# Kernel tuning notes

Measured on AMD Instinct MI355X. Metric: run time of the kernel, lower is better.

## Reference

```python
import jax, jax.numpy as jnp
import numpy as np

EPS_BN = 1e-5
EPS_ENT = 1e-15


def _gcn(x, src, dst, ew, W, b):
    # GCNConv: add self-loops (weight 1), symmetric deg^-1/2 normalization, aggregate x@W.
    n = x.shape[0]
    h = x @ W
    loop = jnp.arange(n)
    s2 = jnp.concatenate([src, loop])
    d2 = jnp.concatenate([dst, loop])
    we2 = jnp.concatenate([ew, jnp.ones((n,), x.dtype)])
    deg = jax.ops.segment_sum(we2, d2, num_segments=n)
    dinv = jnp.where(deg > 0, jax.lax.rsqrt(jnp.maximum(deg, 1e-12)), 0.0)
    coef = dinv[s2] * we2 * dinv[d2]
    return jax.ops.segment_sum(h[s2] * coef[:, None], d2, num_segments=n) + b


def _bn(x, g, be):
    # BatchNorm over the node dimension (training-mode batch stats)
    m = jnp.mean(x, axis=0)
    v = jnp.var(x, axis=0)
    return (x - m) * jax.lax.rsqrt(v + EPS_BN) * g + be


def _block(x, src, dst, ew, W, b, g, be):
    return jax.nn.silu(_bn(_gcn(x, src, dst, ew, W, b), g, be))


def _stoch_pool(x, src, dst, ew, Wp, bp, gp, bep):
    # DiffPool-style: soft cluster assignments from a ResidualBlock, pooled features/adjacency,
    # link loss ||A - S S^T||_F / N^2 (computed sparsely) and mean assignment entropy.
    n = x.shape[0]
    s = jax.nn.softmax(_block(x, src, dst, ew, Wp, bp, gp, bep), axis=-1)  # [n, K]
    K = s.shape[1]
    xp = s.T @ x  # [K, C]
    sw = s[src] * ew[:, None]  # [E, K]
    a_pool = sw.T @ s[dst]  # [K, K] = S^T A S
    cross = jnp.trace(a_pool)  # <A, S S^T>
    sts = s.T @ s  # [K, K]; ||S S^T||_F^2 = ||S^T S||_F^2
    link = jnp.sqrt(jnp.maximum(jnp.sum(ew * ew) - 2.0 * cross + jnp.sum(sts * sts), 0.0)) / (n * n)
    ent = jnp.mean(jnp.sum(-s * jnp.log(s + EPS_ENT), axis=-1))
    grid = jnp.arange(K)
    src_n = jnp.repeat(grid, K)
    dst_n = jnp.tile(grid, K)
    return xp, src_n, dst_n, a_pool.reshape(-1), link, ent


def _level(x, src, dst, ew, Wa, ba, ga, bea, Wb, bb, gb, beb, Wp, bp, gp, bep):
    x = _block(x, src, dst, ew, Wa, ba, ga, bea)
    x = x + _block(x, src, dst, ew, Wb, bb, gb, beb)  # pool_after-1 = 1 residual block
    return _stoch_pool(x, src, dst, ew, Wp, bp, gp, bep)


def setup_inputs() -> dict:
    key = jax.random.key(0)
    ks = jax.random.split(key, 10)
    N, E, IN, CH, K1, K2, OUT = 20000, 640000, 128, 128, 256, 64, 10
    lin = lambda k, fi, fo: (jax.random.normal(k, (fi, fo), jnp.float32) / np.sqrt(fi)).astype(jnp.float32)
    z = lambda c: jnp.zeros((c,), jnp.float32)
    o = lambda c: jnp.ones((c,), jnp.float32)
    d = {
        'x': jax.random.normal(ks[0], (N, IN), jnp.float32),
        'edge_index': jax.random.randint(ks[1], (2, E), 0, N, jnp.int32),
        'batch': jnp.zeros((N,), jnp.int32),
        'batch_ptr': jnp.array([0, N], jnp.int32),
        'W1a': lin(ks[2], IN, CH), 'b1a': z(CH), 'g1a': o(CH), 'be1a': z(CH),
        'W1b': lin(ks[3], CH, CH), 'b1b': z(CH), 'g1b': o(CH), 'be1b': z(CH),
        'Wp1': lin(ks[4], CH, K1), 'bp1': z(K1), 'gp1': o(K1), 'bep1': z(K1),
        'W2a': lin(ks[5], CH, CH), 'b2a': z(CH), 'g2a': o(CH), 'be2a': z(CH),
        'W2b': lin(ks[6], CH, CH), 'b2b': z(CH), 'g2b': o(CH), 'be2b': z(CH),
        'Wp2': lin(ks[7], CH, K2), 'bp2': z(K2), 'gp2': o(K2), 'bep2': z(K2),
        'Wlin': lin(ks[8], CH, OUT), 'blin': z(OUT),
    }
    return d


def reference(x, edge_index, batch, batch_ptr,
              W1a, b1a, g1a, be1a, W1b, b1b, g1b, be1b, Wp1, bp1, gp1, bep1,
              W2a, b2a, g2a, be2a, W2b, b2b, g2b, be2b, Wp2, bp2, gp2, bep2,
              Wlin, blin):
    src, dst = edge_index[0], edge_index[1]
    ew = jnp.ones(src.shape, x.dtype)  # level-1 edge_weight is None -> ones
    x, src, dst, ew, l1, e1 = _level(x, src, dst, ew, W1a, b1a, g1a, be1a,
                                     W1b, b1b, g1b, be1b, Wp1, bp1, gp1, bep1)
    x, src, dst, ew, l2, e2 = _level(x, src, dst, ew, W2a, b2a, g2a, be2a,
                                     W2b, b2b, g2b, be2b, Wp2, bp2, gp2, bep2)
    pooled = jnp.mean(x, axis=0, keepdims=True)  # global_mean_pool, single graph (B=1)
    logits = pooled @ Wlin + blin
    return jax.nn.log_softmax(logits, axis=1), (e1 + e2) + (l1 + l2)
```

## Files before the change

### kernel.cpp

```cpp
#include <hip/hip_runtime.h>

#define EPS_BN 1e-5f
typedef unsigned int uint;
typedef unsigned short ushort;
typedef __attribute__((ext_vector_type(8))) short bf16x8;
typedef __attribute__((ext_vector_type(4))) float f32x4;

__device__ inline ushort f2bf(float f) {
  uint u = __float_as_uint(f);
  uint r = (u + 0x7FFFu + ((u >> 16) & 1u)) >> 16;
  return (ushort)r;
}
__device__ inline float bflo(uint h) { return __uint_as_float(h << 16); }
__device__ inline float bfhi(uint h) { return __uint_as_float(h & 0xFFFF0000u); }


__global__ void k_pre(const int* __restrict__ dst, int* __restrict__ cnt, int E,
                      const float* __restrict__ x, ushort* __restrict__ xb, int n4, int HB) {
  int b = blockIdx.x;
  if (b < HB) {
    int e = b * 256 + threadIdx.x;
    if (e < E) atomicAdd(&cnt[dst[e]], 1);
  } else {
    int i = (b - HB) * 256 + threadIdx.x;
    if (i < n4) {
      float4 v = ((const float4*)x)[i];
      ushort4 o;
      o.x = f2bf(v.x); o.y = f2bf(v.y); o.z = f2bf(v.z); o.w = f2bf(v.w);
      ((ushort4*)xb)[i] = o;
    }
  }
}

__global__ __launch_bounds__(256) void k_scan_par(
    const int* __restrict__ cnt, int* __restrict__ rowptr, int* __restrict__ cursor,
    float* __restrict__ dinv, int* __restrict__ flags, int* __restrict__ partials,
    int N, int E) {
  __shared__ int wsum[4];
  __shared__ int sbase;
  int tile = blockIdx.x;
  int t = threadIdx.x;
  int lane = t & 63, w = t >> 6;
  int i0 = tile * 1024 + t * 4;
  int c[4];
#pragma unroll
  for (int j = 0; j < 4; ++j) {
    int i = i0 + j;
    c[j] = (i < N) ? cnt[i] : 0;
  }
  int p1 = c[0], p2 = p1 + c[1], p3 = p2 + c[2];
  int tsum = p3 + c[3];
  int incl = tsum;
  for (int o = 1; o < 64; o <<= 1) {
    int v = __shfl_up(incl, o);
    if (lane >= o) incl += v;
  }
  int excl = incl - tsum;
  if (lane == 63) wsum[w] = incl;
  __syncthreads();
  if (t == 0) {
    int tot = wsum[0] + wsum[1] + wsum[2] + wsum[3];
    int basev = 0;
    if (tile > 0) {
      while (atomicAdd(&flags[tile - 1], 0) == 0) {}
      basev = atomicAdd(&partials[tile - 1], 0);
    }
    atomicExch(&partials[tile], basev + tot);
    __threadfence();
    atomicExch(&flags[tile], 1);
    sbase = basev;
  }
  __syncthreads();
  int base = sbase;
  for (int ww = 0; ww < w; ++ww) base += wsum[ww];
  base += excl;
  int pre[4] = {0, p1, p2, p3};
#pragma unroll
  for (int j = 0; j < 4; ++j) {
    int i = i0 + j;
    if (i < N) {
      int run = base + pre[j];
      rowptr[i] = run; cursor[i] = run;
      dinv[i] = rsqrtf(1.0f + (float)c[j]);
    }
  }
  if (tile == 0 && t == 0) rowptr[N] = E;
}

__global__ void k_fill_csr(const int* __restrict__ key, const int* __restrict__ val,
                           int* __restrict__ cursor, int* __restrict__ col, int E) {
  int e = blockIdx.x * blockDim.x + threadIdx.x;
  if (e < E) {
    int pos = atomicAdd(&cursor[key[e]], 1);
    col[pos] = val[e];
  }
}


__global__ void k_gather_agg_b2(const int* __restrict__ rowptr, const int* __restrict__ col,
                                const float* __restrict__ dinv, const ushort* __restrict__ H,
                                float* __restrict__ out, int C2) {
  int d = blockIdx.x;
  int c2 = threadIdx.x;
  const uint* H2 = (const uint*)H;
  int b = rowptr[d], e = rowptr[d + 1];
  float a0 = 0.f, a1 = 0.f;
#pragma unroll 4
  for (int i = b; i < e; ++i) {
    int s = col[i];
    float dv = dinv[s];
    uint h = H2[(size_t)s * C2 + c2];
    a0 += dv * bflo(h);
    a1 += dv * bfhi(h);
  }
  float dd = dinv[d];
  uint hd = H2[(size_t)d * C2 + c2];
  float2 o;
  o.x = dd * a0 + dd * dd * bflo(hd);
  o.y = dd * a1 + dd * dd * bfhi(hd);
  *(float2*)(out + (size_t)d * (C2 * 2) + c2 * 2) = o;
}

__global__ void k_gather_agg_b2b(const int* __restrict__ rowptr, const int* __restrict__ col,
                                 const float* __restrict__ dinv, const ushort* __restrict__ H,
                                 ushort* __restrict__ out, int C2) {
  int d = blockIdx.x;
  int c2 = threadIdx.x;
  const uint* H2 = (const uint*)H;
  int b = rowptr[d], e = rowptr[d + 1];
  float a0 = 0.f, a1 = 0.f;
#pragma unroll 4
  for (int i = b; i < e; ++i) {
    int s = col[i];
    float dv = dinv[s];
    uint h = H2[(size_t)s * C2 + c2];
    a0 += dv * bflo(h);
    a1 += dv * bfhi(h);
  }
  float dd = dinv[d];
  uint hd = H2[(size_t)d * C2 + c2];
  ushort2 o;
  o.x = f2bf(dd * a0 + dd * dd * bflo(hd));
  o.y = f2bf(dd * a1 + dd * dd * bfhi(hd));
  *(ushort2*)(out + (size_t)d * (C2 * 2) + c2 * 2) = o;
}

__global__ void k_gather_T_b2b(const int* __restrict__ rowptr, const int* __restrict__ col,
                               const ushort* __restrict__ S, ushort* __restrict__ T, int C2) {
  int s = blockIdx.x;
  int c2 = threadIdx.x;
  const uint* S2 = (const uint*)S;
  int b = rowptr[s], e = rowptr[s + 1];
  float a0 = 0.f, a1 = 0.f;
#pragma unroll 4
  for (int i = b; i < e; ++i) {
    int d = col[i];
    uint h = S2[(size_t)d * C2 + c2];
    a0 += bflo(h);
    a1 += bfhi(h);
  }
  ushort2 o; o.x = f2bf(a0); o.y = f2bf(a1);
  *(ushort2*)(T + (size_t)s * (C2 * 2) + c2 * 2) = o;
}


__global__ void k_tconv(const float* __restrict__ in, ushort* __restrict__ out,
                        int R, int Cc) {
  __shared__ float tile[32][33];
  int c0 = blockIdx.x * 32, r0 = blockIdx.y * 32;
  int tx = threadIdx.x, ty = threadIdx.y;
  for (int i = 0; i < 32; i += 8) {
    int r = r0 + ty + i, c = c0 + tx;
    if (r < R && c < Cc) tile[ty + i][tx] = in[(size_t)r * Cc + c];
  }
  __syncthreads();
  for (int i = 0; i < 32; i += 8) {
    int oc = c0 + ty + i;
    int orr = r0 + tx;
    if (oc < Cc && orr < R) out[(size_t)oc * R + orr] = f2bf(tile[tx][ty + i]);
  }
}

__global__ void k_tconv_b(const ushort* __restrict__ in, ushort* __restrict__ out,
                          int R, int Cc) {
  __shared__ ushort tile[32][33];
  int c0 = blockIdx.x * 32, r0 = blockIdx.y * 32;
  int tx = threadIdx.x, ty = threadIdx.y;
  for (int i = 0; i < 32; i += 8) {
    int r = r0 + ty + i, c = c0 + tx;
    if (r < R && c < Cc) tile[ty + i][tx] = in[(size_t)r * Cc + c];
  }
  __syncthreads();
  for (int i = 0; i < 32; i += 8) {
    int oc = c0 + ty + i;
    int orr = r0 + tx;
    if (oc < Cc && orr < R) out[(size_t)oc * R + orr] = tile[tx][ty + i];
  }
}

__global__ void k_tconv3(const float* __restrict__ W0, const float* __restrict__ W1,
                         const float* __restrict__ W2,
                         ushort* __restrict__ O0, ushort* __restrict__ O1,
                         ushort* __restrict__ O2, int K1) {
  __shared__ float tile[32][33];
  int z = blockIdx.z;
  const float* in = (z == 0) ? W0 : (z == 1) ? W1 : W2;
  ushort* out = (z == 0) ? O0 : (z == 1) ? O1 : O2;
  int Cc = (z == 2) ? K1 : 128;
  int R = 128;
  int c0 = blockIdx.x * 32, r0 = blockIdx.y * 32;
  if (c0 >= Cc) return;
  int tx = threadIdx.x, ty = threadIdx.y;
  for (int i = 0; i < 32; i += 8) {
    int r = r0 + ty + i, c = c0 + tx;
    if (r < R && c < Cc) tile[ty + i][tx] = in[(size_t)r * Cc + c];
  }
  __syncthreads();
  for (int i = 0; i < 32; i += 8) {
    int oc = c0 + ty + i;
    int orr = r0 + tx;
    if (oc < Cc && orr < R) out[(size_t)oc * R + orr] = f2bf(tile[tx][ty + i]);
  }
}

__global__ __launch_bounds__(256) void k_mfma_nt(
    const ushort* __restrict__ A, const ushort* __restrict__ B, float* __restrict__ C,
    ushort* __restrict__ Cb, int I, int J, int K, int kChunk, int atom) {
  __shared__ ushort As[64][40];
  __shared__ ushort Bs[64][40];
  int t = threadIdx.x;
  int w = t >> 6, l = t & 63;
  int i0 = blockIdx.y * 64, j0 = blockIdx.x * 64;
  int k0 = blockIdx.z * kChunk;
  int k1 = min(k0 + kChunk, K);
  f32x4 acc[4] = {};
  int lrow = t >> 2;
  int lk = (t & 3) * 8;
  for (int kk = k0; kk < k1; kk += 32) {
    uint4 av = make_uint4(0u, 0u, 0u, 0u);
    int ar = i0 + lrow;
    if (ar < I) av = *(const uint4*)(A + (size_t)ar * K + kk + lk);
    uint4 bv = *(const uint4*)(B + (size_t)(j0 + lrow) * K + kk + lk);
    *(uint4*)&As[lrow][lk] = av;
    *(uint4*)&Bs[lrow][lk] = bv;
    __syncthreads();
    bf16x8 af = *(const bf16x8*)&As[16 * w + (l & 15)][(l >> 4) * 8];
#pragma unroll
    for (int jt = 0; jt < 4; ++jt) {
      bf16x8 bf = *(const bf16x8*)&Bs[16 * jt + (l & 15)][(l >> 4) * 8];
      acc[jt] = __builtin_amdgcn_mfma_f32_16x16x32_bf16(af, bf, acc[jt], 0, 0, 0);
    }
    __syncthreads();
  }
  int rbase = i0 + 16 * w + ((l >> 4) * 4);
  int cbase = j0 + (l & 15);
#pragma unroll
  for (int jt = 0; jt < 4; ++jt) {
#pragma unroll
    for (int rr = 0; rr < 4; ++rr) {
      int r = rbase + rr;
      if (r < I) {
        size_t idx = (size_t)r * J + jt * 16 + cbase;
        if (Cb) Cb[idx] = f2bf(acc[jt][rr]);
        else if (atom) atomicAdd(&C[idx], acc[jt][rr]);
        else C[idx] = acc[jt][rr];
      }
    }
  }
}

__global__ __launch_bounds__(256) void k_mfma3(
    const ushort* __restrict__ St, const ushort* __restrict__ ATSt,
    const ushort* __restrict__ R2t,
    float* __restrict__ apT, float* __restrict__ sts, float* __restrict__ xp,
    int K, int kChunk) {
  __shared__ ushort As[64][40];
  __shared__ ushort Bs[64][40];
  int xb_ = blockIdx.x;
  const ushort* B; float* C; int J, j0;
  if (xb_ < 4)      { B = ATSt; C = apT; J = 256; j0 = xb_ * 64; }
  else if (xb_ < 8) { B = St;   C = sts; J = 256; j0 = (xb_ - 4) * 64; }
  else              { B = R2t;  C = xp;  J = 128; j0 = (xb_ - 8) * 64; }
  int t = threadIdx.x;
  int w = t >> 6, l = t & 63;
  int i0 = blockIdx.y * 64;
  int k0 = blockIdx.z * kChunk;
  int k1 = min(k0 + kChunk, K);
  f32x4 acc[4] = {};
  int lrow = t >> 2;
  int lk = (t & 3) * 8;
  for (int kk = k0; kk < k1; kk += 32) {
    uint4 av = *(const uint4*)(St + (size_t)(i0 + lrow) * K + kk + lk);
    uint4 bv = *(const uint4*)(B + (size_t)(j0 + lrow) * K + kk + lk);
    *(uint4*)&As[lrow][lk] = av;
    *(uint4*)&Bs[lrow][lk] = bv;
    __syncthreads();
    bf16x8 af = *(const bf16x8*)&As[16 * w + (l & 15)][(l >> 4) * 8];
#pragma unroll
    for (int jt = 0; jt < 4; ++jt) {
      bf16x8 bf = *(const bf16x8*)&Bs[16 * jt + (l & 15)][(l >> 4) * 8];
      acc[jt] = __builtin_amdgcn_mfma_f32_16x16x32_bf16(af, bf, acc[jt], 0, 0, 0);
    }
    __syncthreads();
  }
  int rbase = i0 + 16 * w + ((l >> 4) * 4);
  int cbase = j0 + (l & 15);
#pragma unroll
  for (int jt = 0; jt < 4; ++jt) {
#pragma unroll
    for (int rr = 0; rr < 4; ++rr) {
      atomicAdd(&C[(size_t)(rbase + rr) * J + jt * 16 + cbase], acc[jt][rr]);
    }
  }
}

__global__ __launch_bounds__(256) void k_sgemm_nn(
    const float* __restrict__ A, const float* __restrict__ B, float* __restrict__ C,
    int M, int N, int K) {
  __shared__ float As[16][64];
  __shared__ float Bs[16][68];
  int t = threadIdx.x;
  int tx = t & 15, ty = t >> 4;
  int row0 = blockIdx.y * 64, col0 = blockIdx.x * 64;
  float acc[4][4] = {};
  for (int k0 = 0; k0 < K; k0 += 16) {
    int ar = t >> 2;
    int ak = (t & 3) * 4;
    float4 av = make_float4(0.f, 0.f, 0.f, 0.f);
    if (row0 + ar < M) av = *(const float4*)(A + (size_t)(row0 + ar) * K + k0 + ak);
    As[ak + 0][ar] = av.x; As[ak + 1][ar] = av.y;
    As[ak + 2][ar] = av.z; As[ak + 3][ar] = av.w;
    int bk = t >> 4;
    int bc = (t & 15) * 4;
    float4 bv = *(const float4*)(B + (size_t)(k0 + bk) * N + col0 + bc);
    *(float4*)&Bs[bk][bc] = bv;
    __syncthreads();
#pragma unroll
    for (int k = 0; k < 16; ++k) {
      float a[4], b[4];
#pragma unroll
      for (int u = 0; u < 4; ++u) a[u] = As[k][ty * 4 + u];
#pragma unroll
      for (int v = 0; v < 4; ++v) b[v] = Bs[k][tx * 4 + v];
#pragma unroll
      for (int u = 0; u < 4; ++u)
#pragma unroll
        for (int v = 0; v < 4; ++v) acc[u][v] += a[u] * b[v];
    }
    __syncthreads();
  }
#pragma unroll
  for (int u = 0; u < 4; ++u) {
    int r = row0 + ty * 4 + u;
    if (r < M) {
#pragma unroll
      for (int v = 0; v < 4; ++v) C[(size_t)r * N + col0 + tx * 4 + v] = acc[u][v];
    }
  }
}


__global__ void k_col_stats2(const float* __restrict__ X, const float* __restrict__ bias,
                             float* __restrict__ part, int M, int C, int rpb) {
  int c = threadIdx.x;
  int b = blockIdx.x;
  int r0 = b * rpb, r1 = min(r0 + rpb, M);
  float bi = bias[c];
  float s = 0.f, sq = 0.f;
  for (int r = r0; r < r1; ++r) {
    float v = X[(size_t)r * C + c] + bi;
    s += v; sq += v * v;
  }
  part[(size_t)b * 2 * C + c] = s;
  part[(size_t)b * 2 * C + C + c] = sq;
}

__global__ __launch_bounds__(256) void k_colred_par(
    const float* __restrict__ part, int nblk, int C,
    float* __restrict__ cs, float* __restrict__ csq) {
  __shared__ float sh[256];
  int c = blockIdx.x;
  int t = threadIdx.x;
  float s = 0.f, sq = 0.f;
  for (int b = t; b < nblk; b += 256) {
    s  += part[(size_t)b * 2 * C + c];
    sq += part[(size_t)b * 2 * C + C + c];
  }
  sh[t] = s; __syncthreads();
  for (int o = 128; o > 0; o >>= 1) { if (t < o) sh[t] += sh[t + o]; __syncthreads(); }
  if (t == 0) cs[c] = sh[0];
  __syncthreads();
  sh[t] = sq; __syncthreads();
  for (int o = 128; o > 0; o >>= 1) { if (t < o) sh[t] += sh[t + o]; __syncthreads(); }
  if (t == 0) csq[c] = sh[0];
}

__global__ void k_bn_silu(const float* __restrict__ X, const float* __restrict__ bias,
                          const float* __restrict__ cs, const float* __restrict__ csq,
                          const float* __restrict__ g, const float* __restrict__ be,
                          const float* __restrict__ resid, float* __restrict__ out,
                          ushort* __restrict__ outb,
                          int tot, int cmask, float invM) {
  int i = blockIdx.x * blockDim.x + threadIdx.x;
  if (i >= tot) return;
  int c = i & cmask;
  float m = cs[c] * invM;
  float var = csq[c] * invM - m * m;
  float v = (X[i] + bias[c] - m) * rsqrtf(var + EPS_BN) * g[c] + be[c];
  float y = v / (1.f + expf(-v));
  if (resid) y += resid[i];
  out[i] = y;
  if (outb) outb[i] = f2bf(y);
}

__global__ __launch_bounds__(256) void k_bn_small(
    const float* __restrict__ X, const float* __restrict__ bias,
    const float* __restrict__ g, const float* __restrict__ be,
    const float* __restrict__ resid, float* __restrict__ out,
    int M, int C, float invM) {
  __shared__ float sh[256];
  int c = blockIdx.x;
  int t = threadIdx.x;
  bool act = t < M;
  float v = 0.f;
  if (act) v = X[(size_t)t * C + c] + bias[c];
  sh[t] = v; __syncthreads();
  for (int o = 128; o > 0; o >>= 1) { if (t < o) sh[t] += sh[t + o]; __syncthreads(); }
  float m = sh[0] * invM; __syncthreads();
  sh[t] = v * v; __syncthreads();
  for (int o = 128; o > 0; o >>= 1) { if (t < o) sh[t] += sh[t + o]; __syncthreads(); }
  float var = sh[0] * invM - m * m;
  if (act) {
    float y = (v - m) * rsqrtf(var + EPS_BN) * g[c] + be[c];
    y = y / (1.f + expf(-y));
    if (resid) y += resid[(size_t)t * C + c];
    out[(size_t)t * C + c] = y;
  }
}

template <int C>
__global__ void k_softmax_ent3(float* __restrict__ X, ushort* __restrict__ outb,
                               float* __restrict__ part, int nrows, int writeX) {
  constexpr int VPT = C / 64;
  __shared__ float went[4];
  int gt = blockIdx.x * blockDim.x + threadIdx.x;
  int row = gt >> 6;
  int l = gt & 63;
  int wid = threadIdx.x >> 6;
  bool active = row < nrows;
  size_t base = active ? (size_t)row * C : 0;
  float d[VPT];
  if (VPT == 4) {
    float4 v = *(const float4*)(X + base + l * 4);
    d[0] = v.x; d[1] = v.y; d[2] = v.z; d[3] = v.w;
  } else {
    d[0] = X[base + l];
  }
  float mx = d[0];
#pragma unroll
  for (int i = 1; i < VPT; ++i) mx = fmaxf(mx, d[i]);
  for (int o = 32; o > 0; o >>= 1) mx = fmaxf(mx, __shfl_xor(mx, o));
  float se = 0.f;
  float e[VPT];
#pragma unroll
  for (int i = 0; i < VPT; ++i) { d[i] -= mx; e[i] = expf(d[i]); se += e[i]; }
  for (int o = 32; o > 0; o >>= 1) se += __shfl_xor(se, o);
  float inv = 1.f / se;
  float pd = 0.f;
#pragma unroll
  for (int i = 0; i < VPT; ++i) { e[i] *= inv; pd += e[i] * d[i]; }
  if (active) {
    if (VPT == 4) {
      if (writeX) {
        float4 v; v.x = e[0]; v.y = e[1]; v.z = e[2]; v.w = e[3];
        *(float4*)(X + base + l * 4) = v;
      }
      if (outb) {
        ushort4 u; u.x = f2bf(e[0]); u.y = f2bf(e[1]); u.z = f2bf(e[2]); u.w = f2bf(e[3]);
        *(ushort4*)(outb + base + l * 4) = u;
      }
    } else {
      if (writeX) X[base + l] = e[0];
      if (outb) outb[base + l] = f2bf(e[0]);
    }
  }
  for (int o = 32; o > 0; o >>= 1) pd += __shfl_xor(pd, o);
  if (l == 0) went[wid] = active ? (logf(se) - pd) : 0.f;
  __syncthreads();
  if (threadIdx.x == 0) part[blockIdx.x] = went[0] + went[1] + went[2] + went[3];
}

__global__ __launch_bounds__(256) void k_reduce_atom(
    const float* __restrict__ in, int n, float* __restrict__ out) {
  __shared__ float sh[256];
  int t = threadIdx.x;
  int per = (n + gridDim.x - 1) / gridDim.x;
  int i0 = blockIdx.x * per, i1 = min(i0 + per, n);
  float s = 0.f;
  for (int i = i0 + t; i < i1; i += 256) s += in[i];
  sh[t] = s; __syncthreads();
  for (int o = 128; o > 0; o >>= 1) { if (t < o) sh[t] += sh[t + o]; __syncthreads(); }
  if (t == 0) atomicAdd(out, sh[0]);
}

__global__ __launch_bounds__(256) void k_scalN_par(
    const float* __restrict__ P0, const float* __restrict__ P1, int K,
    float* __restrict__ outb, int Z) {
  __shared__ float sh[256];
  int b = blockIdx.x, t = threadIdx.x;
  float s = 0.f;
  int slot;
  if (b == 0) {
    slot = 0;
    for (int i = t; i < K; i += 256) s += P0[(size_t)i * K + i];
  } else {
    int which = (b - 1) / Z;
    int chunk = (b - 1) % Z;
    slot = 1 + which;
    const float4* P4 = (const float4*)(which ? P0 : P1);
    int n4 = (K * K) >> 2;
    int per = (n4 + Z - 1) / Z;
    int i0 = chunk * per, i1 = min(i0 + per, n4);
    for (int i = i0 + t; i < i1; i += 256) {
      float4 v = P4[i];
      s += v.x * v.x + v.y * v.y + v.z * v.z + v.w * v.w;
    }
  }
  sh[t] = s; __syncthreads();
  for (int o = 128; o > 0; o >>= 1) { if (t < o) sh[t] += sh[t + o]; __syncthreads(); }
  if (t == 0) atomicAdd(&outb[slot], sh[0]);
}

__global__ __launch_bounds__(256) void k_scal2_par(
    const float* __restrict__ U, const float* __restrict__ V, int n,
    const float* __restrict__ P, int nP, float* __restrict__ outb, int Z) {
  __shared__ float sh[256];
  int b = blockIdx.x, t = threadIdx.x;
  float s = 0.f;
  int slot;
  if (b < Z) {
    slot = 0;
    const float4* U4 = (const float4*)U;
    const float4* V4 = (const float4*)V;
    int n4 = n >> 2;
    int per = (n4 + Z - 1) / Z;
    int i0 = b * per, i1 = min(i0 + per, n4);
    for (int i = i0 + t; i < i1; i += 256) {
      float4 u = U4[i], v = V4[i];
      s += u.x * v.x + u.y * v.y + u.z * v.z + u.w * v.w;
    }
  } else {
    slot = 1;
    const float4* P4 = (const float4*)P;
    int n4 = nP >> 2;
    for (int i = t; i < n4; i += 256) {
      float4 v = P4[i];
      s += v.x * v.x + v.y * v.y + v.z * v.z + v.w * v.w;
    }
  }
  sh[t] = s; __syncthreads();
  for (int o = 128; o > 0; o >>= 1) { if (t < o) sh[t] += sh[t + o]; __syncthreads(); }
  if (t == 0) atomicAdd(&outb[slot], sh[0]);
}


__global__ __launch_bounds__(256) void k_deg2_par(
    const float* __restrict__ A2T, float* __restrict__ dinv2, int Np) {
  __shared__ float sh[256];
  int q = blockIdx.x;
  int t = threadIdx.x;
  float s = (t == 0) ? 1.0f : 0.f;
  for (int p = t; p < Np; p += 256) s += A2T[(size_t)q * Np + p];
  sh[t] = s; __syncthreads();
  for (int o = 128; o > 0; o >>= 1) { if (t < o) sh[t] += sh[t + o]; __syncthreads(); }
  if (t == 0) {
    float d = sh[0];
    dinv2[q] = d > 0.f ? rsqrtf(fmaxf(d, 1e-12f)) : 0.f;
  }
}

__global__ void k_dense_agg(const float* __restrict__ A2T, const float* __restrict__ dinv2,
                            const float* __restrict__ H, float* __restrict__ out,
                            int Np, int C) {
  int q = blockIdx.x, c = threadIdx.x;
  float acc = 0.f;
#pragma unroll 8
  for (int p = 0; p < Np; ++p)
    acc += dinv2[p] * A2T[(size_t)q * Np + p] * H[(size_t)p * C + c];
  float dq = dinv2[q];
  out[(size_t)q * C + c] = dq * acc + dq * dq * H[(size_t)q * C + c];
}

__global__ __launch_bounds__(256) void k_tn3(
    const float* __restrict__ S, const float* __restrict__ B2,
    float* __restrict__ sts2, float* __restrict__ xp2, int M) {
  __shared__ float As[64][65];
  __shared__ float Bs[64][65];
  int z = blockIdx.x;
  const float* B; float* C; int J, j0;
  if (z == 0) { B = S;  C = sts2; J = 64;  j0 = 0; }
  else        { B = B2; C = xp2;  J = 128; j0 = (z - 1) * 64; }
  int t = threadIdx.x;
  int tj = t & 63, ti = t >> 6;
  float acc[16] = {};
  for (int m0 = 0; m0 < M; m0 += 64) {
#pragma unroll
    for (int r = 0; r < 16; ++r) {
      As[ti * 16 + r][tj] = S[(size_t)(m0 + ti * 16 + r) * 64 + tj];
      Bs[ti * 16 + r][tj] = B[(size_t)(m0 + ti * 16 + r) * J + j0 + tj];
    }
    __syncthreads();
#pragma unroll 4
    for (int mm = 0; mm < 64; ++mm) {
      float bv = Bs[mm][tj];
#pragma unroll
      for (int ii = 0; ii < 16; ++ii) acc[ii] += As[mm][ti * 16 + ii] * bv;
    }
    __syncthreads();
  }
  for (int ii = 0; ii < 16; ++ii) C[(size_t)(ti * 16 + ii) * J + j0 + tj] = acc[ii];
}

__global__ void k_final(const float* __restrict__ xp2, const float* __restrict__ Wlin,
                        const float* __restrict__ blin, const float* __restrict__ scal,
                        float* __restrict__ out, int N1, int E1, int K1, int K2, int OUT) {
  __shared__ float pooled[128];
  __shared__ float logits[32];
  int t = threadIdx.x;
  float s = 0.f;
  for (int r = 0; r < K2; ++r) s += xp2[(size_t)r * 128 + t];
  pooled[t] = s / (float)K2;
  __syncthreads();
  if (t < OUT) {
    float acc = blin[t];
    for (int k = 0; k < 128; ++k) acc += pooled[k] * Wlin[(size_t)k * OUT + t];
    logits[t] = acc;
  }
  __syncthreads();
  if (t == 0) {
    float mx = logits[0];
    for (int j = 1; j < OUT; ++j) mx = fmaxf(mx, logits[j]);
    float se = 0.f;
    for (int j = 0; j < OUT; ++j) se += expf(logits[j] - mx);
    float lse = mx + logf(se);
    for (int j = 0; j < OUT; ++j) out[j] = logits[j] - lse;
    float n1 = (float)N1;
    float ent1 = scal[0] / n1;
    float ent2 = scal[1] / (float)K1;
    float link1 = sqrtf(fmaxf((float)E1 - 2.f * scal[2] + scal[3], 0.f)) / (n1 * n1);
    float link2 = sqrtf(fmaxf(scal[4] - 2.f * scal[5] + scal[6], 0.f)) / ((float)K1 * (float)K1);
    out[OUT] = ent1 + ent2 + link1 + link2;
  }
}


extern "C" void kernel_launch(void* const* d_in, const int* in_sizes, int n_in,
                              void* d_out, int out_size, void* d_ws, size_t ws_size,
                              hipStream_t stream) {
  (void)n_in; (void)out_size; (void)ws_size;
  const float* x = (const float*)d_in[0];
  const int* ei  = (const int*)d_in[1];
  const int N = in_sizes[0] / 128;
  const int E = in_sizes[1] / 2;
  const int* src = ei;
  const int* dst = ei + E;
  const float *W1a=(const float*)d_in[4],  *b1a=(const float*)d_in[5],
              *g1a=(const float*)d_in[6],  *be1a=(const float*)d_in[7];
  const float *W1b=(const float*)d_in[8],  *b1b=(const float*)d_in[9],
              *g1b=(const float*)d_in[10], *be1b=(const float*)d_in[11];
  const float *Wp1=(const float*)d_in[12], *bp1=(const float*)d_in[13],
              *gp1=(const float*)d_in[14], *bep1=(const float*)d_in[15];
  const float *W2a=(const float*)d_in[16], *b2a=(const float*)d_in[17],
              *g2a=(const float*)d_in[18], *be2a=(const float*)d_in[19];
  const float *W2b=(const float*)d_in[20], *b2b=(const float*)d_in[21],
              *g2b=(const float*)d_in[22], *be2b=(const float*)d_in[23];
  const float *Wp2=(const float*)d_in[24], *bp2=(const float*)d_in[25],
              *gp2=(const float*)d_in[26], *bep2=(const float*)d_in[27];
  const float *Wlin=(const float*)d_in[28], *blin=(const float*)d_in[29];
  const int K1 = in_sizes[12] / 128;
  const int K2 = in_sizes[24] / 128;
  const int OUT = in_sizes[29];

  char* base = (char*)d_ws;
  size_t off = 0;
  auto allocb = [&](size_t bytes) -> void* {
    void* p = (void*)(base + off);
    off += ((bytes + 255) & ~(size_t)255);
    return p;
  };
  auto alloc = [&](size_t nf) -> float* { return (float*)allocb(nf * 4); };
  auto alloci = [&](size_t ni) -> int* { return (int*)allocb(ni * 4); };
  auto allocu = [&](size_t nu) -> ushort* { return (ushort*)allocb(nu * 2); };

  auto cdiv = [](long long a, long long b) { return (int)((a + b - 1) / b); };

  const int RPB = 16;
  const int NBLK1 = cdiv(N, RPB);
  const int NTILES = cdiv(N, 1024);

  float* scal  = alloc(16);
  float* cs    = alloc(256);
  float* csq   = alloc(256);
  float* dinv  = alloc(N);
  float* dinv2 = alloc(K1);
  float* apT   = alloc((size_t)K1 * K1);
  float* sts   = alloc((size_t)K1 * K1);
  float* xp    = alloc((size_t)K1 * 128);
  float* h2    = alloc((size_t)K1 * 128);
  float* y2    = alloc((size_t)K1 * 128);
  float* xa2   = alloc((size_t)K1 * 128);
  float* x2f   = alloc((size_t)K1 * 128);
  float* s2b   = alloc((size_t)K1 * K2);
  float* U     = alloc((size_t)K1 * K2);
  float* sts2  = alloc((size_t)K2 * K2);
  float* xp2   = alloc((size_t)K2 * 128);
  float* ent1p = alloc(cdiv(N, 4) + 8);
  float* ent2p = alloc(64 + 8);
  float* csp   = alloc((size_t)(NBLK1 + 2) * 512);
  float* R1 = alloc((size_t)N * 128);
  float* R2 = alloc((size_t)N * 128);
  float* R3 = alloc((size_t)N * K1);
  float* R4 = alloc((size_t)N * K1);
  ushort* B16A = allocu((size_t)N * 128);
  ushort* W1at = allocu(128 * 128);
  ushort* W1bt = allocu(128 * 128);
  ushort* Wp1t = allocu((size_t)K1 * 128);
  int* cnt_d = alloci((size_t)N + 64);
  int* flags = cnt_d + N;
  int* parts = cnt_d + N + 32;
  int* rp_d  = alloci(N + 1);
  int* cur_d = alloci(N);
  int* col_s = alloci(E);

  ushort* Hb   = (ushort*)R3;
  ushort* aggB = (ushort*)R3;
  ushort* Sb   = (ushort*)R3;
  ushort* ATSb = (ushort*)R4;
  ushort* St   = (ushort*)R1;
  ushort* ATSt = (ushort*)R2;
  ushort* R2t  = B16A;

  hipMemsetAsync(scal, 0, 16 * sizeof(float), stream);

  hipMemsetAsync(cnt_d, 0, ((size_t)N + 64) * sizeof(int), stream);
  {
    int HB = cdiv(E, 256);
    int CB = cdiv((size_t)N * 128 / 4, 256);
    k_pre<<<HB + CB, 256, 0, stream>>>(dst, cnt_d, E, x, B16A, N * 128 / 4, HB);
  }
  k_scan_par<<<NTILES, 256, 0, stream>>>(cnt_d, rp_d, cur_d, dinv, flags, parts, N, E);
  k_fill_csr<<<cdiv(E, 256), 256, 0, stream>>>(dst, src, cur_d, col_s, E);

  {
    dim3 b32(32, 8);
    k_tconv3<<<dim3(8, 4, 3), b32, 0, stream>>>(W1a, W1b, Wp1, W1at, W1bt, Wp1t, K1);
  }

  auto mfma_nt = [&](const ushort* A, const ushort* B, float* C, ushort* Cb,
                     int I, int J, int K) {
    dim3 g(J / 64, cdiv(I, 64), 1);
    k_mfma_nt<<<g, 256, 0, stream>>>(A, B, C, Cb, I, J, K, K, 0);
  };
  auto gemm_nn = [&](const float* A, const float* B, float* C, int M, int Nn, int K) {
    dim3 g(Nn / 64, cdiv(M, 64));
    k_sgemm_nn<<<g, 256, 0, stream>>>(A, B, C, M, Nn, K);
  };

  auto block1 = [&](const ushort* xin_b, const ushort* Wt, const float* b, const float* gg,
                    const float* be, const float* resid, float* outp, ushort* outb, int C) {
    mfma_nt(xin_b, Wt, nullptr, Hb, N, C, 128);
    k_gather_agg_b2<<<N, C / 2, 0, stream>>>(rp_d, col_s, dinv, Hb, R4, C / 2);
    k_col_stats2<<<NBLK1, C, 0, stream>>>(R4, b, csp, N, C, RPB);
    k_colred_par<<<C, 256, 0, stream>>>(csp, NBLK1, C, cs, csq);
    int tot = N * C;
    k_bn_silu<<<cdiv(tot, 256), 256, 0, stream>>>(R4, b, cs, csq, gg, be, resid, outp,
                                                  outb, tot, C - 1, 1.f / N);
  };

  block1(B16A, W1at, b1a, g1a, be1a, nullptr, R1, B16A, 128);
  block1(B16A, W1bt, b1b, g1b, be1b, R1,      R2, B16A, 128);

  k_gather_agg_b2b<<<N, 64, 0, stream>>>(rp_d, col_s, dinv, B16A, aggB, 64);
  mfma_nt(aggB, Wp1t, R4, nullptr, N, K1, 128);
  k_col_stats2<<<NBLK1, K1, 0, stream>>>(R4, bp1, csp, N, K1, RPB);
  k_colred_par<<<K1, 256, 0, stream>>>(csp, NBLK1, K1, cs, csq);
  k_bn_silu<<<cdiv(N * K1, 256), 256, 0, stream>>>(R4, bp1, cs, csq, gp1, bep1, nullptr,
                                                   R4, nullptr, N * K1, K1 - 1, 1.f / N);
  k_softmax_ent3<256><<<cdiv(N, 4), 256, 0, stream>>>(R4, Sb, ent1p, N, 0);
  k_reduce_atom<<<8, 256, 0, stream>>>(ent1p, cdiv(N, 4), &scal[0]);

  {
    dim3 b32(32, 8);
    k_tconv_b<<<dim3(K1 / 32, cdiv(N, 32)), b32, 0, stream>>>(Sb, St, N, K1);
    k_tconv<<<dim3(128 / 32, cdiv(N, 32)), b32, 0, stream>>>(R2, R2t, N, 128);
  }
  k_gather_T_b2b<<<N, K1 / 2, 0, stream>>>(rp_d, col_s, Sb, ATSb, K1 / 2);
  {
    dim3 b32(32, 8);
    k_tconv_b<<<dim3(K1 / 32, cdiv(N, 32)), b32, 0, stream>>>(ATSb, ATSt, N, K1);
  }

  {
    hipMemsetAsync(apT, 0, (size_t)(2 * K1 * K1 + K1 * 128) * sizeof(float), stream);
    int chunk = ((cdiv(N, 16) + 31) & ~31);
    int z = cdiv(N, chunk);
    k_mfma3<<<dim3(10, 4, z), 256, 0, stream>>>(St, ATSt, R2t, apT, sts, xp, N, chunk);
  }
  k_scalN_par<<<1 + 2 * 16, 256, 0, stream>>>(apT, sts, K1, &scal[2], 16);

  k_deg2_par<<<K1, 256, 0, stream>>>(apT, dinv2, K1);

  auto block2 = [&](const float* xin, const float* W, const float* b, const float* gg,
                    const float* be, const float* resid, float* outp, int C) {
    gemm_nn(xin, W, h2, K1, C, 128);
    k_dense_agg<<<K1, C, 0, stream>>>(apT, dinv2, h2, y2, K1, C);
    k_bn_small<<<C, 256, 0, stream>>>(y2, b, gg, be, resid, outp, K1, C, 1.f / K1);
  };

  block2(xp,  W2a, b2a, g2a, be2a, nullptr, xa2, 128);
  block2(xa2, W2b, b2b, g2b, be2b, xa2,     x2f, 128);
  block2(x2f, Wp2, bp2, gp2, bep2, nullptr, s2b, K2);
  k_softmax_ent3<64><<<cdiv(K1, 4), 256, 0, stream>>>(s2b, nullptr, ent2p, K1, 1);
  k_reduce_atom<<<2, 256, 0, stream>>>(ent2p, cdiv(K1, 4), &scal[1]);

  gemm_nn(apT, s2b, U, K1, K2, K1);
  k_tn3<<<3, 256, 0, stream>>>(s2b, x2f, sts2, xp2, K1);
  k_scal2_par<<<8 + 1, 256, 0, stream>>>(U, s2b, K1 * K2, sts2, K2 * K2, &scal[5], 8);

  k_final<<<1, 128, 0, stream>>>(xp2, Wlin, blin, scal, (float*)d_out, N, E, K1, K2, OUT);
}
```

Measured before the change: 519.7 us.

## Keep level-1 activations in bf16 and fuse pool BN-SiLU into softmax

```diff
diff --git a/kernel.cpp b/kernel.cpp
--- a/kernel.cpp
+++ b/kernel.cpp
@@ -13,6 +13,7 @@
 }
 __device__ inline float bflo(uint h) { return __uint_as_float(h << 16); }
 __device__ inline float bfhi(uint h) { return __uint_as_float(h & 0xFFFF0000u); }
+__device__ inline float bf2f(ushort h) { return __uint_as_float(((uint)h) << 16); }
 
 
 __global__ void k_pre(const int* __restrict__ dst, int* __restrict__ cnt, int E,
@@ -163,23 +164,6 @@
   *(ushort2*)(T + (size_t)s * (C2 * 2) + c2 * 2) = o;
 }
 
-
-__global__ void k_tconv(const float* __restrict__ in, ushort* __restrict__ out,
-                        int R, int Cc) {
-  __shared__ float tile[32][33];
-  int c0 = blockIdx.x * 32, r0 = blockIdx.y * 32;
-  int tx = threadIdx.x, ty = threadIdx.y;
-  for (int i = 0; i < 32; i += 8) {
-    int r = r0 + ty + i, c = c0 + tx;
-    if (r < R && c < Cc) tile[ty + i][tx] = in[(size_t)r * Cc + c];
-  }
-  __syncthreads();
-  for (int i = 0; i < 32; i += 8) {
-    int oc = c0 + ty + i;
-    int orr = r0 + tx;
-    if (oc < Cc && orr < R) out[(size_t)oc * R + orr] = f2bf(tile[tx][ty + i]);
-  }
-}
 
 __global__ void k_tconv_b(const ushort* __restrict__ in, ushort* __restrict__ out,
                           int R, int Cc) {
@@ -375,6 +359,21 @@
   part[(size_t)b * 2 * C + C + c] = sq;
 }
 
+__global__ void k_col_stats2b(const ushort* __restrict__ X, const float* __restrict__ bias,
+                              float* __restrict__ part, int M, int C, int rpb) {
+  int c = threadIdx.x;
+  int b = blockIdx.x;
+  int r0 = b * rpb, r1 = min(r0 + rpb, M);
+  float bi = bias[c];
+  float s = 0.f, sq = 0.f;
+  for (int r = r0; r < r1; ++r) {
+    float v = bf2f(X[(size_t)r * C + c]) + bi;
+    s += v; sq += v * v;
+  }
+  part[(size_t)b * 2 * C + c] = s;
+  part[(size_t)b * 2 * C + C + c] = sq;
+}
+
 __global__ __launch_bounds__(256) void k_colred_par(
     const float* __restrict__ part, int nblk, int C,
     float* __restrict__ cs, float* __restrict__ csq) {
@@ -398,8 +397,7 @@
 __global__ void k_bn_silu(const float* __restrict__ X, const float* __restrict__ bias,
                           const float* __restrict__ cs, const float* __restrict__ csq,
                           const float* __restrict__ g, const float* __restrict__ be,
-                          const float* __restrict__ resid, float* __restrict__ out,
-                          ushort* __restrict__ outb,
+                          const ushort* __restrict__ residb, ushort* __restrict__ outb,
                           int tot, int cmask, float invM) {
   int i = blockIdx.x * blockDim.x + threadIdx.x;
   if (i >= tot) return;
@@ -408,9 +406,8 @@
   float var = csq[c] * invM - m * m;
   float v = (X[i] + bias[c] - m) * rsqrtf(var + EPS_BN) * g[c] + be[c];
   float y = v / (1.f + expf(-v));
-  if (resid) y += resid[i];
-  out[i] = y;
-  if (outb) outb[i] = f2bf(y);
+  if (residb) y += bf2f(residb[i]);
+  outb[i] = f2bf(y);
 }
 
 __global__ __launch_bounds__(256) void k_bn_small(
@@ -439,8 +436,55 @@
 }
 
 template <int C>
-__global__ void k_softmax_ent3(float* __restrict__ X, ushort* __restrict__ outb,
-                               float* __restrict__ part, int nrows, int writeX) {
+__global__ void k_bn_softmax(const ushort* __restrict__ H, const float* __restrict__ bias,
+                             const float* __restrict__ cs, const float* __restrict__ csq,
+                             const float* __restrict__ g, const float* __restrict__ be,
+                             ushort* __restrict__ outb, float* __restrict__ part,
+                             int nrows, float invM) {
+  constexpr int VPT = C / 64;
+  __shared__ float went[4];
+  int gt = blockIdx.x * blockDim.x + threadIdx.x;
+  int row = gt >> 6;
+  int l = gt & 63;
+  int wid = threadIdx.x >> 6;
+  bool active = row < nrows;
+  size_t base = active ? (size_t)row * C : 0;
+  ushort4 hv = *(const ushort4*)(H + base + l * 4);
+  ushort hs[4] = {hv.x, hv.y, hv.z, hv.w};
+  float d[VPT];
+#pragma unroll
+  for (int i = 0; i < VPT; ++i) {
+    int c = l * 4 + i;
+    float m = cs[c] * invM;
+    float var = csq[c] * invM - m * m;
+    float v = (bf2f(hs[i]) + bias[c] - m) * rsqrtf(var + EPS_BN) * g[c] + be[c];
+    d[i] = v / (1.f + expf(-v));
+  }
+  float mx = d[0];
+#pragma unroll
+  for (int i = 1; i < VPT; ++i) mx = fmaxf(mx, d[i]);
+  for (int o = 32; o > 0; o >>= 1) mx = fmaxf(mx, __shfl_xor(mx, o));
+  float se = 0.f;
+  float e[VPT];
+#pragma unroll
+  for (int i = 0; i < VPT; ++i) { d[i] -= mx; e[i] = expf(d[i]); se += e[i]; }
+  for (int o = 32; o > 0; o >>= 1) se += __shfl_xor(se, o);
+  float inv = 1.f / se;
+  float pd = 0.f;
+#pragma unroll
+  for (int i = 0; i < VPT; ++i) { e[i] *= inv; pd += e[i] * d[i]; }
+  if (active) {
+    ushort4 u; u.x = f2bf(e[0]); u.y = f2bf(e[1]); u.z = f2bf(e[2]); u.w = f2bf(e[3]);
+    *(ushort4*)(outb + base + l * 4) = u;
+  }
+  for (int o = 32; o > 0; o >>= 1) pd += __shfl_xor(pd, o);
+  if (l == 0) went[wid] = active ? (logf(se) - pd) : 0.f;
+  __syncthreads();
+  if (threadIdx.x == 0) part[blockIdx.x] = went[0] + went[1] + went[2] + went[3];
+}
+
+template <int C>
+__global__ void k_softmax_ent3(float* __restrict__ X, float* __restrict__ part, int nrows) {
   constexpr int VPT = C / 64;
   __shared__ float went[4];
   int gt = blockIdx.x * blockDim.x + threadIdx.x;
@@ -450,15 +494,8 @@
   bool active = row < nrows;
   size_t base = active ? (size_t)row * C : 0;
   float d[VPT];
-  if (VPT == 4) {
-    float4 v = *(const float4*)(X + base + l * 4);
-    d[0] = v.x; d[1] = v.y; d[2] = v.z; d[3] = v.w;
-  } else {
-    d[0] = X[base + l];
-  }
+  d[0] = X[base + l];
   float mx = d[0];
-#pragma unroll
-  for (int i = 1; i < VPT; ++i) mx = fmaxf(mx, d[i]);
   for (int o = 32; o > 0; o >>= 1) mx = fmaxf(mx, __shfl_xor(mx, o));
   float se = 0.f;
   float e[VPT];
@@ -469,21 +506,7 @@
   float pd = 0.f;
 #pragma unroll
   for (int i = 0; i < VPT; ++i) { e[i] *= inv; pd += e[i] * d[i]; }
-  if (active) {
-    if (VPT == 4) {
-      if (writeX) {
-        float4 v; v.x = e[0]; v.y = e[1]; v.z = e[2]; v.w = e[3];
-        *(float4*)(X + base + l * 4) = v;
-      }
-      if (outb) {
-        ushort4 u; u.x = f2bf(e[0]); u.y = f2bf(e[1]); u.z = f2bf(e[2]); u.w = f2bf(e[3]);
-        *(ushort4*)(outb + base + l * 4) = u;
-      }
-    } else {
-      if (writeX) X[base + l] = e[0];
-      if (outb) outb[base + l] = f2bf(e[0]);
-    }
-  }
+  if (active) X[base + l] = e[0];
   for (int o = 32; o > 0; o >>= 1) pd += __shfl_xor(pd, o);
   if (l == 0) went[wid] = active ? (logf(se) - pd) : 0.f;
   __syncthreads();
@@ -722,6 +745,7 @@
   float* R3 = alloc((size_t)N * K1);
   float* R4 = alloc((size_t)N * K1);
   ushort* B16A = allocu((size_t)N * 128);
+  ushort* R2tb = allocu((size_t)N * 128);
   ushort* W1at = allocu(128 * 128);
   ushort* W1bt = allocu(128 * 128);
   ushort* Wp1t = allocu((size_t)K1 * 128);
@@ -735,10 +759,10 @@
   ushort* Hb   = (ushort*)R3;
   ushort* aggB = (ushort*)R3;
   ushort* Sb   = (ushort*)R3;
+  ushort* Pb   = (ushort*)R4;
   ushort* ATSb = (ushort*)R4;
   ushort* St   = (ushort*)R1;
   ushort* ATSt = (ushort*)R2;
-  ushort* R2t  = B16A;
 
   hipMemsetAsync(scal, 0, 16 * sizeof(float), stream);
 
@@ -766,33 +790,32 @@
     k_sgemm_nn<<<g, 256, 0, stream>>>(A, B, C, M, Nn, K);
   };
 
-  auto block1 = [&](const ushort* xin_b, const ushort* Wt, const float* b, const float* gg,
-                    const float* be, const float* resid, float* outp, ushort* outb, int C) {
-    mfma_nt(xin_b, Wt, nullptr, Hb, N, C, 128);
-    k_gather_agg_b2<<<N, C / 2, 0, stream>>>(rp_d, col_s, dinv, Hb, R4, C / 2);
-    k_col_stats2<<<NBLK1, C, 0, stream>>>(R4, b, csp, N, C, RPB);
-    k_colred_par<<<C, 256, 0, stream>>>(csp, NBLK1, C, cs, csq);
-    int tot = N * C;
-    k_bn_silu<<<cdiv(tot, 256), 256, 0, stream>>>(R4, b, cs, csq, gg, be, resid, outp,
-                                                  outb, tot, C - 1, 1.f / N);
+  auto block1 = [&](const float* b, const float* gg, const float* be,
+                    const ushort* Wt, const ushort* residb) {
+    mfma_nt(B16A, Wt, nullptr, Hb, N, 128, 128);
+    k_gather_agg_b2<<<N, 64, 0, stream>>>(rp_d, col_s, dinv, Hb, R4, 64);
+    k_col_stats2<<<NBLK1, 128, 0, stream>>>(R4, b, csp, N, 128, RPB);
+    k_colred_par<<<128, 256, 0, stream>>>(csp, NBLK1, 128, cs, csq);
+    int tot = N * 128;
+    k_bn_silu<<<cdiv(tot, 256), 256, 0, stream>>>(R4, b, cs, csq, gg, be, residb, B16A,
+                                                  tot, 127, 1.f / N);
   };
 
-  block1(B16A, W1at, b1a, g1a, be1a, nullptr, R1, B16A, 128);
-  block1(B16A, W1bt, b1b, g1b, be1b, R1,      R2, B16A, 128);
+  block1(b1a, g1a, be1a, W1at, nullptr);
+  block1(b1b, g1b, be1b, W1bt, B16A);
 
   k_gather_agg_b2b<<<N, 64, 0, stream>>>(rp_d, col_s, dinv, B16A, aggB, 64);
-  mfma_nt(aggB, Wp1t, R4, nullptr, N, K1, 128);
-  k_col_stats2<<<NBLK1, K1, 0, stream>>>(R4, bp1, csp, N, K1, RPB);
+  mfma_nt(aggB, Wp1t, nullptr, Pb, N, K1, 128);
+  k_col_stats2b<<<NBLK1, K1, 0, stream>>>(Pb, bp1, csp, N, K1, RPB);
   k_colred_par<<<K1, 256, 0, stream>>>(csp, NBLK1, K1, cs, csq);
-  k_bn_silu<<<cdiv(N * K1, 256), 256, 0, stream>>>(R4, bp1, cs, csq, gp1, bep1, nullptr,
-                                                   R4, nullptr, N * K1, K1 - 1, 1.f / N);
-  k_softmax_ent3<256><<<cdiv(N, 4), 256, 0, stream>>>(R4, Sb, ent1p, N, 0);
+  k_bn_softmax<256><<<cdiv(N, 4), 256, 0, stream>>>(Pb, bp1, cs, csq, gp1, bep1,
+                                                    Sb, ent1p, N, 1.f / N);
   k_reduce_atom<<<8, 256, 0, stream>>>(ent1p, cdiv(N, 4), &scal[0]);
 
   {
     dim3 b32(32, 8);
     k_tconv_b<<<dim3(K1 / 32, cdiv(N, 32)), b32, 0, stream>>>(Sb, St, N, K1);
-    k_tconv<<<dim3(128 / 32, cdiv(N, 32)), b32, 0, stream>>>(R2, R2t, N, 128);
+    k_tconv_b<<<dim3(128 / 32, cdiv(N, 32)), b32, 0, stream>>>(B16A, R2tb, N, 128);
   }
   k_gather_T_b2b<<<N, K1 / 2, 0, stream>>>(rp_d, col_s, Sb, ATSb, K1 / 2);
   {
@@ -804,7 +827,7 @@
     hipMemsetAsync(apT, 0, (size_t)(2 * K1 * K1 + K1 * 128) * sizeof(float), stream);
     int chunk = ((cdiv(N, 16) + 31) & ~31);
     int z = cdiv(N, chunk);
-    k_mfma3<<<dim3(10, 4, z), 256, 0, stream>>>(St, ATSt, R2t, apT, sts, xp, N, chunk);
+    k_mfma3<<<dim3(10, 4, z), 256, 0, stream>>>(St, ATSt, R2tb, apT, sts, xp, N, chunk);
   }
   k_scalN_par<<<1 + 2 * 16, 256, 0, stream>>>(apT, sts, K1, &scal[2], 16);
 
@@ -820,7 +843,7 @@
   block2(xp,  W2a, b2a, g2a, be2a, nullptr, xa2, 128);
   block2(xa2, W2b, b2b, g2b, be2b, xa2,     x2f, 128);
   block2(x2f, Wp2, bp2, gp2, bep2, nullptr, s2b, K2);
-  k_softmax_ent3<64><<<cdiv(K1, 4), 256, 0, stream>>>(s2b, nullptr, ent2p, K1, 1);
+  k_softmax_ent3<64><<<cdiv(K1, 4), 256, 0, stream>>>(s2b, ent2p, K1);
   k_reduce_atom<<<2, 256, 0, stream>>>(ent2p, cdiv(K1, 4), &scal[1]);
 
   gemm_nn(apT, s2b, U, K1, K2, K1);
```

Result: no change. 515.4 us (-0.8%).
